# Optimization experiments

Measured on AMD Instinct MI355X. Metric: run time of the kernel, lower is better.

The kernel has to match this reference:

```python
import jax, jax.numpy as jnp
import numpy as np

BATCH = 2048
INPUT_DIM = 256
NUM_SUBCARRIERS = 256
HIDDEN_DIM = 256


def setup_inputs() -> dict:
    key = jax.random.key(0)
    ks = jax.random.split(key, 7)
    C, I, H = NUM_SUBCARRIERS, INPUT_DIM, HIDDEN_DIM
    # PyTorch nn.Linear default init: U(-1/sqrt(fan_in), 1/sqrt(fan_in))
    s1 = 1.0 / np.sqrt(I)
    s2 = 1.0 / np.sqrt(H)
    x = jax.random.normal(ks[0], (BATCH, I), dtype=jnp.float32)
    W1 = jax.random.uniform(ks[1], (C, I, H), jnp.float32, -s1, s1)
    b1 = jax.random.uniform(ks[2], (C, H), jnp.float32, -s1, s1)
    W2 = jax.random.uniform(ks[3], (C, H, H), jnp.float32, -s2, s2)
    b2 = jax.random.uniform(ks[4], (C, H), jnp.float32, -s2, s2)
    W3 = jax.random.uniform(ks[5], (C, H), jnp.float32, -s2, s2)  # [C, H] (out dim 1 squeezed)
    b3 = jax.random.uniform(ks[6], (C,), jnp.float32, -s2, s2)
    return {"x": x, "W1": W1, "b1": b1, "W2": W2, "b2": b2, "W3": W3, "b3": b3}


def reference(x, W1, b1, W2, b2, W3, b3):
    # Stacked (batched) version of the per-subcarrier Python loop:
    # for each subcarrier c: relu(relu(x @ W1[c] + b1[c]) @ W2[c] + b2[c]) @ W3[c] + b3[c]
    h1 = jax.nn.relu(jnp.einsum('bi,cih->cbh', x, W1) + b1[:, None, :])   # [C, B, H]
    h2 = jax.nn.relu(jnp.einsum('cbh,chk->cbk', h1, W2) + b2[:, None, :])  # [C, B, H]
    out = jnp.einsum('cbh,ch->cb', h2, W3) + b3[:, None]                   # [C, B]
    return out.T  # [B, C], matches torch.cat(outputs, dim=1)
```

## Files before the change

### kernel.cpp

```cpp
#include <hip/hip_runtime.h>

typedef unsigned short u16;
using u16x4  = __attribute__((ext_vector_type(4))) unsigned short;
using u16x8  = __attribute__((ext_vector_type(8))) unsigned short;
using bf16x8 = __attribute__((ext_vector_type(8))) short;
using f32x4  = __attribute__((ext_vector_type(4))) float;
using f32x16 = __attribute__((ext_vector_type(16))) float;

__device__ __forceinline__ u16 f2bf(float f) {
  union { float f; unsigned u; } v; v.f = f;
  unsigned r = v.u + 0x7FFFu + ((v.u >> 16) & 1u);
  return (u16)(r >> 16);
}

__device__ __forceinline__ unsigned cvt_pk_bf16(float a, float b) {
  unsigned d;
  asm("v_cvt_pk_bf16_f32 %0, %1, %2" : "=v"(d) : "v"(a), "v"(b));
  return d;
}

__global__ void convert_x_k(const float* __restrict__ in, u16* __restrict__ out) {
  int i = blockIdx.x * 256 + threadIdx.x;
  float4 v = ((const float4*)in)[i];
  u16x4 u;
  u.x = f2bf(v.x); u.y = f2bf(v.y); u.z = f2bf(v.z); u.w = f2bf(v.w);
  ((u16x4*)out)[i] = u;
}

__global__ __launch_bounds__(256) void transpose_w2_k(
    const float* __restrict__ W1, const float* __restrict__ W2,
    u16* __restrict__ w1t, u16* __restrict__ w2t) {
  __shared__ float tile[64][65];
  const int bid = blockIdx.x;
  const int mat = bid >> 4;
  const int tl  = bid & 15;
  const int i0 = (tl >> 2) * 64, h0 = (tl & 3) * 64;
  const float* src = (mat < 256) ? (W1 + mat * 65536) : (W2 + (mat - 256) * 65536);
  u16*       dst   = (mat < 256) ? (w1t + mat * 65536) : (w2t + (mat - 256) * 65536);
  const int t = threadIdx.x;
#pragma unroll
  for (int j = 0; j < 4; ++j) {
    int lin = j * 256 + t;
    int row = lin >> 4, c4 = lin & 15;
    float4 v = *(const float4*)(src + (i0 + row) * 256 + h0 + c4 * 4);
    tile[row][c4 * 4 + 0] = v.x; tile[row][c4 * 4 + 1] = v.y;
    tile[row][c4 * 4 + 2] = v.z; tile[row][c4 * 4 + 3] = v.w;
  }
  __syncthreads();
  const int col = t >> 2;
  const int kk  = (t & 3) * 8;
#pragma unroll
  for (int p = 0; p < 2; ++p) {
    u16x8 o;
#pragma unroll
    for (int jj = 0; jj < 8; ++jj)
      o[jj] = f2bf(tile[p * 32 + kk + jj][col]);
    *(u16x8*)(dst + ((i0 >> 4) + 2 * p + (kk >> 4)) * 4096 + (h0 + col) * 16 + (kk & 8)) = o;
  }
}

__global__ __launch_bounds__(512, 4) void rf_main_k(
    const u16* __restrict__ xb, const u16* __restrict__ w1t, const u16* __restrict__ w2t,
    const float* __restrict__ b1, const float* __restrict__ b2,
    const float* __restrict__ w3, const float* __restrict__ b3,
    float* __restrict__ out) {
  __shared__ u16 sH[128 * 264];
  __shared__ float red[8 * 128];

  const int bid  = blockIdx.x;
  const int xcd  = bid & 7;
  const int j8   = bid >> 3;
  const int c    = xcd * 32 + (j8 >> 4);
  const int b0   = (j8 & 15) * 128;
  const int t    = threadIdx.x;
  const int lane = t & 63;
  const int w    = t >> 6;
  const int l31  = lane & 31;
  const int hi   = lane >> 5;
  const bool hiH = hi != 0;
  const int wq   = w & 3;
  const int bh   = w >> 2;
  const int m_base = wq * 64;
  const int n_base = bh * 64;

  const u16* w1c = w1t + c * 65536;
  const u16* w2c = w2t + c * 65536;
  const int aoff = (m_base + l31) * 16 + hi * 8;
  const int bbase = (n_base + l31) * 264 + hi * 8;
  const int bidx = __builtin_amdgcn_readfirstlane(c * 256 + m_base);

  f32x16 acc[2][2];
  bf16x8 aA[2], aB[2];

#define LOADA(dst, base)                                         \
  { dst[0] = *(const bf16x8*)(base);                             \
    dst[1] = *(const bf16x8*)((base) + 512); }

#define COMPUTE(fr, ch)                                          \
  { bf16x8 _b0 = *(const bf16x8*)&sH[bbase + (ch) * 16];         \
    bf16x8 _b1 = *(const bf16x8*)&sH[bbase + (ch) * 16 + 8448];  \
    acc[0][0] = __builtin_amdgcn_mfma_f32_32x32x16_bf16(fr[0], _b0, acc[0][0], 0, 0, 0); \
    acc[1][0] = __builtin_amdgcn_mfma_f32_32x32x16_bf16(fr[1], _b0, acc[1][0], 0, 0, 0); \
    acc[0][1] = __builtin_amdgcn_mfma_f32_32x32x16_bf16(fr[0], _b1, acc[0][1], 0, 0, 0); \
    acc[1][1] = __builtin_amdgcn_mfma_f32_32x32x16_bf16(fr[1], _b1, acc[1][1], 0, 0, 0); }

#define INIT_ACC(bp)                                             \
  { _Pragma("unroll")                                            \
    for (int _mi = 0; _mi < 2; ++_mi) {                          \
      _Pragma("unroll")                                          \
      for (int _g = 0; _g < 4; ++_g) {                           \
        f32x4 _lo = *(const f32x4*)((bp) + bidx + _mi * 32 + _g * 8);     \
        f32x4 _h4 = *(const f32x4*)((bp) + bidx + _mi * 32 + _g * 8 + 4); \
        _Pragma("unroll")                                        \
        for (int _r = 0; _r < 4; ++_r) {                         \
          float _v = hiH ? _h4[_r] : _lo[_r];                    \
          acc[_mi][0][_g * 4 + _r] = _v;                         \
          acc[_mi][1][_g * 4 + _r] = _v;                         \
        } } } }

  LOADA(aA, w1c + aoff);

#pragma unroll
  for (int i = 0; i < 8; ++i) {
    int flat = i * 512 + t;
    int r = flat >> 5, s = flat & 31;
    u16x8 g = *(const u16x8*)(xb + (b0 + r) * 256 + s * 8);
    *(u16x8*)&sH[r * 264 + s * 8] = g;
  }
  INIT_ACC(b1);
  __syncthreads();

#pragma unroll 1
  for (int ch = 0; ch < 16; ch += 2) {
    LOADA(aB, w1c + (ch + 1) * 4096 + aoff);
    COMPUTE(aA, ch);
    const u16* nxt = (ch == 14) ? (w2c + aoff)
                                : (w1c + (ch + 2) * 4096 + aoff);
    LOADA(aA, nxt);
    COMPUTE(aB, ch + 1);
  }

  __syncthreads();
#pragma unroll
  for (int mi = 0; mi < 2; ++mi)
#pragma unroll
    for (int nj = 0; nj < 2; ++nj) {
      const int row = n_base + nj * 32 + l31;
#pragma unroll
      for (int g = 0; g < 4; ++g) {
        float v0 = fmaxf(acc[mi][nj][g * 4 + 0], 0.f);
        float v1 = fmaxf(acc[mi][nj][g * 4 + 1], 0.f);
        float v2 = fmaxf(acc[mi][nj][g * 4 + 2], 0.f);
        float v3 = fmaxf(acc[mi][nj][g * 4 + 3], 0.f);
        uint2 p;
        p.x = cvt_pk_bf16(v0, v1);
        p.y = cvt_pk_bf16(v2, v3);
        *(uint2*)&sH[row * 264 + m_base + mi * 32 + g * 8 + 4 * hi] = p;
      }
    }
  INIT_ACC(b2);
  __syncthreads();

#pragma unroll 1
  for (int ch = 0; ch < 16; ch += 2) {
    LOADA(aB, w2c + (ch + 1) * 4096 + aoff);
    COMPUTE(aA, ch);
    if (ch < 14) LOADA(aA, w2c + (ch + 2) * 4096 + aoff);
    COMPUTE(aB, ch + 1);
  }

  float part0 = 0.f, part1 = 0.f;
#pragma unroll
  for (int mi = 0; mi < 2; ++mi)
#pragma unroll
    for (int g = 0; g < 4; ++g) {
      f32x4 wlo = *(const f32x4*)(w3 + bidx + mi * 32 + g * 8);
      f32x4 whi = *(const f32x4*)(w3 + bidx + mi * 32 + g * 8 + 4);
#pragma unroll
      for (int r = 0; r < 4; ++r) {
        float wv = hiH ? whi[r] : wlo[r];
        part0 += fmaxf(acc[mi][0][g * 4 + r], 0.f) * wv;
        part1 += fmaxf(acc[mi][1][g * 4 + r], 0.f) * wv;
      }
    }
  red[(wq * 2 + hi) * 128 + n_base + l31]      = part0;
  red[(wq * 2 + hi) * 128 + n_base + 32 + l31] = part1;
  __syncthreads();
  if (t < 128) {
    float v = b3[c];
#pragma unroll
    for (int k = 0; k < 8; ++k) v += red[k * 128 + t];
    out[(b0 + t) * 256 + c] = v;
  }
#undef LOADA
#undef COMPUTE
#undef INIT_ACC
}

extern "C" void kernel_launch(void* const* d_in, const int* in_sizes, int n_in,
                              void* d_out, int out_size, void* d_ws, size_t ws_size,
                              hipStream_t stream) {
  const float* x  = (const float*)d_in[0];
  const float* W1 = (const float*)d_in[1];
  const float* b1 = (const float*)d_in[2];
  const float* W2 = (const float*)d_in[3];
  const float* b2 = (const float*)d_in[4];
  const float* W3 = (const float*)d_in[5];
  const float* b3 = (const float*)d_in[6];
  float* out = (float*)d_out;

  char* ws = (char*)d_ws;
  u16* xb  = (u16*)ws;
  u16* w1t = (u16*)(ws + (1u << 20));
  u16* w2t = (u16*)(ws + (1u << 20) + (32u << 20));

  convert_x_k   <<<512,  256, 0, stream>>>(x,  xb);
  transpose_w2_k<<<8192, 256, 0, stream>>>(W1, W2, w1t, w2t);
  rf_main_k     <<<4096, 512, 0, stream>>>(xb, w1t, w2t, b1, b2, W3, b3, out);
}
```

Baseline: 304.3 us.

## Retile warps to 128x32 output tiles and merge x conversion into weight prepass

Each warp now covers 128 hidden units by 32 batch rows instead of 64x64. It loads four A fragments from global memory and one shared-memory B fragment per step, halving LDS reads for B and the final reduction buffer. This doubles per-warp global A-fragment traffic and register pressure, with the weights reloaded by twice as many warps. Separately, the x conversion kernel is folded into the transpose prepass as extra blocks, which removes one kernel launch.

```diff
diff --git a/kernel.cpp b/kernel.cpp
--- a/kernel.cpp
+++ b/kernel.cpp
@@ -19,25 +19,26 @@
   return d;
 }
 
-__global__ void convert_x_k(const float* __restrict__ in, u16* __restrict__ out) {
-  int i = blockIdx.x * 256 + threadIdx.x;
-  float4 v = ((const float4*)in)[i];
-  u16x4 u;
-  u.x = f2bf(v.x); u.y = f2bf(v.y); u.z = f2bf(v.z); u.w = f2bf(v.w);
-  ((u16x4*)out)[i] = u;
-}
-
-__global__ __launch_bounds__(256) void transpose_w2_k(
+__global__ __launch_bounds__(256) void prepass_k(
     const float* __restrict__ W1, const float* __restrict__ W2,
-    u16* __restrict__ w1t, u16* __restrict__ w2t) {
+    u16* __restrict__ w1t, u16* __restrict__ w2t,
+    const float* __restrict__ x, u16* __restrict__ xb) {
   __shared__ float tile[64][65];
   const int bid = blockIdx.x;
+  const int t = threadIdx.x;
+  if (bid >= 8192) {
+    int i = (bid - 8192) * 256 + t;
+    float4 v = ((const float4*)x)[i];
+    u16x4 u;
+    u.x = f2bf(v.x); u.y = f2bf(v.y); u.z = f2bf(v.z); u.w = f2bf(v.w);
+    ((u16x4*)xb)[i] = u;
+    return;
+  }
   const int mat = bid >> 4;
   const int tl  = bid & 15;
   const int i0 = (tl >> 2) * 64, h0 = (tl & 3) * 64;
   const float* src = (mat < 256) ? (W1 + mat * 65536) : (W2 + (mat - 256) * 65536);
   u16*       dst   = (mat < 256) ? (w1t + mat * 65536) : (w2t + (mat - 256) * 65536);
-  const int t = threadIdx.x;
 #pragma unroll
   for (int j = 0; j < 4; ++j) {
     int lin = j * 256 + t;
@@ -65,7 +66,7 @@
     const float* __restrict__ w3, const float* __restrict__ b3,
     float* __restrict__ out) {
   __shared__ u16 sH[128 * 264];
-  __shared__ float red[8 * 128];
+  __shared__ float red[4 * 128];
 
   const int bid  = blockIdx.x;
   const int xcd  = bid & 7;
@@ -78,10 +79,10 @@
   const int l31  = lane & 31;
   const int hi   = lane >> 5;
   const bool hiH = hi != 0;
-  const int wq   = w & 3;
-  const int bh   = w >> 2;
-  const int m_base = wq * 64;
-  const int n_base = bh * 64;
+  const int wq   = w & 1;
+  const int bh   = w >> 1;
+  const int m_base = wq * 128;
+  const int n_base = bh * 32;
 
   const u16* w1c = w1t + c * 65536;
   const u16* w2c = w2t + c * 65536;
@@ -89,34 +90,32 @@
   const int bbase = (n_base + l31) * 264 + hi * 8;
   const int bidx = __builtin_amdgcn_readfirstlane(c * 256 + m_base);
 
-  f32x16 acc[2][2];
-  bf16x8 aA[2], aB[2];
+  f32x16 acc[4];
+  bf16x8 aA[4], aB[4];
 
 #define LOADA(dst, base)                                         \
-  { dst[0] = *(const bf16x8*)(base);                             \
-    dst[1] = *(const bf16x8*)((base) + 512); }
+  { _Pragma("unroll")                                            \
+    for (int _mi = 0; _mi < 4; ++_mi)                            \
+      dst[_mi] = *(const bf16x8*)((base) + _mi * 512); }
 
 #define COMPUTE(fr, ch)                                          \
-  { bf16x8 _b0 = *(const bf16x8*)&sH[bbase + (ch) * 16];         \
-    bf16x8 _b1 = *(const bf16x8*)&sH[bbase + (ch) * 16 + 8448];  \
-    acc[0][0] = __builtin_amdgcn_mfma_f32_32x32x16_bf16(fr[0], _b0, acc[0][0], 0, 0, 0); \
-    acc[1][0] = __builtin_amdgcn_mfma_f32_32x32x16_bf16(fr[1], _b0, acc[1][0], 0, 0, 0); \
-    acc[0][1] = __builtin_amdgcn_mfma_f32_32x32x16_bf16(fr[0], _b1, acc[0][1], 0, 0, 0); \
-    acc[1][1] = __builtin_amdgcn_mfma_f32_32x32x16_bf16(fr[1], _b1, acc[1][1], 0, 0, 0); }
+  { bf16x8 _b = *(const bf16x8*)&sH[bbase + (ch) * 16];          \
+    acc[0] = __builtin_amdgcn_mfma_f32_32x32x16_bf16(fr[0], _b, acc[0], 0, 0, 0); \
+    acc[1] = __builtin_amdgcn_mfma_f32_32x32x16_bf16(fr[1], _b, acc[1], 0, 0, 0); \
+    acc[2] = __builtin_amdgcn_mfma_f32_32x32x16_bf16(fr[2], _b, acc[2], 0, 0, 0); \
+    acc[3] = __builtin_amdgcn_mfma_f32_32x32x16_bf16(fr[3], _b, acc[3], 0, 0, 0); }
 
 #define INIT_ACC(bp)                                             \
   { _Pragma("unroll")                                            \
-    for (int _mi = 0; _mi < 2; ++_mi) {                          \
+    for (int _mi = 0; _mi < 4; ++_mi) {                          \
       _Pragma("unroll")                                          \
       for (int _g = 0; _g < 4; ++_g) {                           \
         f32x4 _lo = *(const f32x4*)((bp) + bidx + _mi * 32 + _g * 8);     \
         f32x4 _h4 = *(const f32x4*)((bp) + bidx + _mi * 32 + _g * 8 + 4); \
         _Pragma("unroll")                                        \
-        for (int _r = 0; _r < 4; ++_r) {                         \
-          float _v = hiH ? _h4[_r] : _lo[_r];                    \
-          acc[_mi][0][_g * 4 + _r] = _v;                         \
-          acc[_mi][1][_g * 4 + _r] = _v;                         \
-        } } } }
+        for (int _r = 0; _r < 4; ++_r)                           \
+          acc[_mi][_g * 4 + _r] = hiH ? _h4[_r] : _lo[_r];       \
+      } } }
 
   LOADA(aA, w1c + aoff);
 
@@ -141,23 +140,22 @@
   }
 
   __syncthreads();
-#pragma unroll
-  for (int mi = 0; mi < 2; ++mi)
-#pragma unroll
-    for (int nj = 0; nj < 2; ++nj) {
-      const int row = n_base + nj * 32 + l31;
+  {
+    const int row = n_base + l31;
+#pragma unroll
+    for (int mi = 0; mi < 4; ++mi)
 #pragma unroll
       for (int g = 0; g < 4; ++g) {
-        float v0 = fmaxf(acc[mi][nj][g * 4 + 0], 0.f);
-        float v1 = fmaxf(acc[mi][nj][g * 4 + 1], 0.f);
-        float v2 = fmaxf(acc[mi][nj][g * 4 + 2], 0.f);
-        float v3 = fmaxf(acc[mi][nj][g * 4 + 3], 0.f);
+        float v0 = fmaxf(acc[mi][g * 4 + 0], 0.f);
+        float v1 = fmaxf(acc[mi][g * 4 + 1], 0.f);
+        float v2 = fmaxf(acc[mi][g * 4 + 2], 0.f);
+        float v3 = fmaxf(acc[mi][g * 4 + 3], 0.f);
         uint2 p;
         p.x = cvt_pk_bf16(v0, v1);
         p.y = cvt_pk_bf16(v2, v3);
         *(uint2*)&sH[row * 264 + m_base + mi * 32 + g * 8 + 4 * hi] = p;
       }
-    }
+  }
   INIT_ACC(b2);
   __syncthreads();
 
@@ -169,9 +167,9 @@
     COMPUTE(aB, ch + 1);
   }
 
-  float part0 = 0.f, part1 = 0.f;
-#pragma unroll
-  for (int mi = 0; mi < 2; ++mi)
+  float part = 0.f;
+#pragma unroll
+  for (int mi = 0; mi < 4; ++mi)
 #pragma unroll
     for (int g = 0; g < 4; ++g) {
       f32x4 wlo = *(const f32x4*)(w3 + bidx + mi * 32 + g * 8);
@@ -179,17 +177,15 @@
 #pragma unroll
       for (int r = 0; r < 4; ++r) {
         float wv = hiH ? whi[r] : wlo[r];
-        part0 += fmaxf(acc[mi][0][g * 4 + r], 0.f) * wv;
-        part1 += fmaxf(acc[mi][1][g * 4 + r], 0.f) * wv;
+        part += fmaxf(acc[mi][g * 4 + r], 0.f) * wv;
       }
     }
-  red[(wq * 2 + hi) * 128 + n_base + l31]      = part0;
-  red[(wq * 2 + hi) * 128 + n_base + 32 + l31] = part1;
+  red[(wq * 2 + hi) * 128 + n_base + l31] = part;
   __syncthreads();
   if (t < 128) {
     float v = b3[c];
 #pragma unroll
-    for (int k = 0; k < 8; ++k) v += red[k * 128 + t];
+    for (int k = 0; k < 4; ++k) v += red[k * 128 + t];
     out[(b0 + t) * 256 + c] = v;
   }
 #undef LOADA
@@ -214,7 +210,6 @@
   u16* w1t = (u16*)(ws + (1u << 20));
   u16* w2t = (u16*)(ws + (1u << 20) + (32u << 20));
 
-  convert_x_k   <<<512,  256, 0, stream>>>(x,  xb);
-  transpose_w2_k<<<8192, 256, 0, stream>>>(W1, W2, w1t, w2t);
-  rf_main_k     <<<4096, 512, 0, stream>>>(xb, w1t, w2t, b1, b2, W3, b3, out);
-}
+  prepass_k <<<8704, 256, 0, stream>>>(W1, W2, w1t, w2t, x, xb);
+  rf_main_k <<<4096, 512, 0, stream>>>(xb, w1t, w2t, b1, b2, W3, b3, out);
+}
```

Result: slower. 343.0 us (+12.7%).

## Double batch tile per block, prefetch LDS B fragments, merge prepass kernels

Applied to the files above, without the earlier changes.

Each main-kernel block now handles 256 batch rows instead of 128, so each wave computes a 64x128 tile and the per-subcarrier weight fragments are reused across twice as many rows. Global weight traffic and block count are halved. B operands are now double-buffered from LDS in registers ahead of the MFMAs. The x conversion and weight transpose are fused into one launch to drop a kernel launch. Costs: more accumulator registers and LDS per block, which lowers occupancy (launch bounds reduced to 2 blocks per CU).

```diff
diff --git a/kernel.cpp b/kernel.cpp
--- a/kernel.cpp
+++ b/kernel.cpp
@@ -19,25 +19,26 @@
   return d;
 }
 
-__global__ void convert_x_k(const float* __restrict__ in, u16* __restrict__ out) {
-  int i = blockIdx.x * 256 + threadIdx.x;
-  float4 v = ((const float4*)in)[i];
-  u16x4 u;
-  u.x = f2bf(v.x); u.y = f2bf(v.y); u.z = f2bf(v.z); u.w = f2bf(v.w);
-  ((u16x4*)out)[i] = u;
-}
-
-__global__ __launch_bounds__(256) void transpose_w2_k(
+__global__ __launch_bounds__(256) void prepass_k(
     const float* __restrict__ W1, const float* __restrict__ W2,
-    u16* __restrict__ w1t, u16* __restrict__ w2t) {
+    u16* __restrict__ w1t, u16* __restrict__ w2t,
+    const float* __restrict__ x, u16* __restrict__ xb) {
   __shared__ float tile[64][65];
   const int bid = blockIdx.x;
+  const int t = threadIdx.x;
+  if (bid >= 8192) {
+    int i = (bid - 8192) * 256 + t;
+    float4 v = ((const float4*)x)[i];
+    u16x4 u;
+    u.x = f2bf(v.x); u.y = f2bf(v.y); u.z = f2bf(v.z); u.w = f2bf(v.w);
+    ((u16x4*)xb)[i] = u;
+    return;
+  }
   const int mat = bid >> 4;
   const int tl  = bid & 15;
   const int i0 = (tl >> 2) * 64, h0 = (tl & 3) * 64;
   const float* src = (mat < 256) ? (W1 + mat * 65536) : (W2 + (mat - 256) * 65536);
   u16*       dst   = (mat < 256) ? (w1t + mat * 65536) : (w2t + (mat - 256) * 65536);
-  const int t = threadIdx.x;
 #pragma unroll
   for (int j = 0; j < 4; ++j) {
     int lin = j * 256 + t;
@@ -59,19 +60,18 @@
   }
 }
 
-__global__ __launch_bounds__(512, 4) void rf_main_k(
+__global__ __launch_bounds__(512, 2) void rf_main_k(
     const u16* __restrict__ xb, const u16* __restrict__ w1t, const u16* __restrict__ w2t,
     const float* __restrict__ b1, const float* __restrict__ b2,
     const float* __restrict__ w3, const float* __restrict__ b3,
     float* __restrict__ out) {
-  __shared__ u16 sH[128 * 264];
-  __shared__ float red[8 * 128];
+  __shared__ u16 sH[256 * 264];
 
   const int bid  = blockIdx.x;
   const int xcd  = bid & 7;
   const int j8   = bid >> 3;
-  const int c    = xcd * 32 + (j8 >> 4);
-  const int b0   = (j8 & 15) * 128;
+  const int c    = xcd * 32 + (j8 >> 3);
+  const int b0   = (j8 & 7) * 256;
   const int t    = threadIdx.x;
   const int lane = t & 63;
   const int w    = t >> 6;
@@ -81,28 +81,34 @@
   const int wq   = w & 3;
   const int bh   = w >> 2;
   const int m_base = wq * 64;
-  const int n_base = bh * 64;
 
   const u16* w1c = w1t + c * 65536;
   const u16* w2c = w2t + c * 65536;
   const int aoff = (m_base + l31) * 16 + hi * 8;
-  const int bbase = (n_base + l31) * 264 + hi * 8;
+  int bb[4];
+#pragma unroll
+  for (int nj = 0; nj < 4; ++nj)
+    bb[nj] = (bh * 128 + nj * 32 + l31) * 264 + hi * 8;
   const int bidx = __builtin_amdgcn_readfirstlane(c * 256 + m_base);
 
-  f32x16 acc[2][2];
-  bf16x8 aA[2], aB[2];
+  f32x16 acc[2][4];
+  bf16x8 aA[2], aB[2], bX[4], bY[4];
 
 #define LOADA(dst, base)                                         \
   { dst[0] = *(const bf16x8*)(base);                             \
     dst[1] = *(const bf16x8*)((base) + 512); }
 
-#define COMPUTE(fr, ch)                                          \
-  { bf16x8 _b0 = *(const bf16x8*)&sH[bbase + (ch) * 16];         \
-    bf16x8 _b1 = *(const bf16x8*)&sH[bbase + (ch) * 16 + 8448];  \
-    acc[0][0] = __builtin_amdgcn_mfma_f32_32x32x16_bf16(fr[0], _b0, acc[0][0], 0, 0, 0); \
-    acc[1][0] = __builtin_amdgcn_mfma_f32_32x32x16_bf16(fr[1], _b0, acc[1][0], 0, 0, 0); \
-    acc[0][1] = __builtin_amdgcn_mfma_f32_32x32x16_bf16(fr[0], _b1, acc[0][1], 0, 0, 0); \
-    acc[1][1] = __builtin_amdgcn_mfma_f32_32x32x16_bf16(fr[1], _b1, acc[1][1], 0, 0, 0); }
+#define LOADB(dst, ch)                                           \
+  { _Pragma("unroll")                                            \
+    for (int _nj = 0; _nj < 4; ++_nj)                            \
+      dst[_nj] = *(const bf16x8*)&sH[bb[_nj] + (ch) * 16]; }
+
+#define COMPUTE(afr, bfr)                                        \
+  { _Pragma("unroll")                                            \
+    for (int _nj = 0; _nj < 4; ++_nj) {                          \
+      acc[0][_nj] = __builtin_amdgcn_mfma_f32_32x32x16_bf16(afr[0], bfr[_nj], acc[0][_nj], 0, 0, 0); \
+      acc[1][_nj] = __builtin_amdgcn_mfma_f32_32x32x16_bf16(afr[1], bfr[_nj], acc[1][_nj], 0, 0, 0); \
+    } }
 
 #define INIT_ACC(bp)                                             \
   { _Pragma("unroll")                                            \
@@ -114,14 +120,15 @@
         _Pragma("unroll")                                        \
         for (int _r = 0; _r < 4; ++_r) {                         \
           float _v = hiH ? _h4[_r] : _lo[_r];                    \
-          acc[_mi][0][_g * 4 + _r] = _v;                         \
-          acc[_mi][1][_g * 4 + _r] = _v;                         \
+          _Pragma("unroll")                                      \
+          for (int _nj = 0; _nj < 4; ++_nj)                      \
+            acc[_mi][_nj][_g * 4 + _r] = _v;                     \
         } } } }
 
   LOADA(aA, w1c + aoff);
 
 #pragma unroll
-  for (int i = 0; i < 8; ++i) {
+  for (int i = 0; i < 16; ++i) {
     int flat = i * 512 + t;
     int r = flat >> 5, s = flat & 31;
     u16x8 g = *(const u16x8*)(xb + (b0 + r) * 256 + s * 8);
@@ -130,22 +137,25 @@
   INIT_ACC(b1);
   __syncthreads();
 
+  LOADB(bX, 0);
 #pragma unroll 1
   for (int ch = 0; ch < 16; ch += 2) {
     LOADA(aB, w1c + (ch + 1) * 4096 + aoff);
-    COMPUTE(aA, ch);
+    LOADB(bY, ch + 1);
+    COMPUTE(aA, bX);
     const u16* nxt = (ch == 14) ? (w2c + aoff)
                                 : (w1c + (ch + 2) * 4096 + aoff);
     LOADA(aA, nxt);
-    COMPUTE(aB, ch + 1);
-  }
-
-  __syncthreads();
-#pragma unroll
-  for (int mi = 0; mi < 2; ++mi)
-#pragma unroll
-    for (int nj = 0; nj < 2; ++nj) {
-      const int row = n_base + nj * 32 + l31;
+    if (ch < 14) LOADB(bX, ch + 2);
+    COMPUTE(aB, bY);
+  }
+
+  __syncthreads();
+#pragma unroll
+  for (int nj = 0; nj < 4; ++nj) {
+    const int row = bh * 128 + nj * 32 + l31;
+#pragma unroll
+    for (int mi = 0; mi < 2; ++mi)
 #pragma unroll
       for (int g = 0; g < 4; ++g) {
         float v0 = fmaxf(acc[mi][nj][g * 4 + 0], 0.f);
@@ -157,19 +167,24 @@
         p.y = cvt_pk_bf16(v2, v3);
         *(uint2*)&sH[row * 264 + m_base + mi * 32 + g * 8 + 4 * hi] = p;
       }
-    }
+  }
   INIT_ACC(b2);
   __syncthreads();
 
+  LOADB(bX, 0);
 #pragma unroll 1
   for (int ch = 0; ch < 16; ch += 2) {
     LOADA(aB, w2c + (ch + 1) * 4096 + aoff);
-    COMPUTE(aA, ch);
-    if (ch < 14) LOADA(aA, w2c + (ch + 2) * 4096 + aoff);
-    COMPUTE(aB, ch + 1);
-  }
-
-  float part0 = 0.f, part1 = 0.f;
+    LOADB(bY, ch + 1);
+    COMPUTE(aA, bX);
+    if (ch < 14) {
+      LOADA(aA, w2c + (ch + 2) * 4096 + aoff);
+      LOADB(bX, ch + 2);
+    }
+    COMPUTE(aB, bY);
+  }
+
+  float part[4] = {0.f, 0.f, 0.f, 0.f};
 #pragma unroll
   for (int mi = 0; mi < 2; ++mi)
 #pragma unroll
@@ -179,20 +194,25 @@
 #pragma unroll
       for (int r = 0; r < 4; ++r) {
         float wv = hiH ? whi[r] : wlo[r];
-        part0 += fmaxf(acc[mi][0][g * 4 + r], 0.f) * wv;
-        part1 += fmaxf(acc[mi][1][g * 4 + r], 0.f) * wv;
+#pragma unroll
+        for (int nj = 0; nj < 4; ++nj)
+          part[nj] += fmaxf(acc[mi][nj][g * 4 + r], 0.f) * wv;
       }
     }
-  red[(wq * 2 + hi) * 128 + n_base + l31]      = part0;
-  red[(wq * 2 + hi) * 128 + n_base + 32 + l31] = part1;
-  __syncthreads();
-  if (t < 128) {
+  __syncthreads();
+  float* red = (float*)sH;
+#pragma unroll
+  for (int nj = 0; nj < 4; ++nj)
+    red[(wq * 2 + hi) * 256 + bh * 128 + nj * 32 + l31] = part[nj];
+  __syncthreads();
+  if (t < 256) {
     float v = b3[c];
 #pragma unroll
-    for (int k = 0; k < 8; ++k) v += red[k * 128 + t];
+    for (int k = 0; k < 8; ++k) v += red[k * 256 + t];
     out[(b0 + t) * 256 + c] = v;
   }
 #undef LOADA
+#undef LOADB
 #undef COMPUTE
 #undef INIT_ACC
 }
@@ -214,7 +234,6 @@
   u16* w1t = (u16*)(ws + (1u << 20));
   u16* w2t = (u16*)(ws + (1u << 20) + (32u << 20));
 
-  convert_x_k   <<<512,  256, 0, stream>>>(x,  xb);
-  transpose_w2_k<<<8192, 256, 0, stream>>>(W1, W2, w1t, w2t);
-  rf_main_k     <<<4096, 512, 0, stream>>>(xb, w1t, w2t, b1, b2, W3, b3, out);
-}
+  prepass_k <<<8704, 256, 0, stream>>>(W1, W2, w1t, w2t, x, xb);
+  rf_main_k <<<2048, 512, 0, stream>>>(xb, w1t, w2t, b1, b2, W3, b3, out);
+}
```

After: 302.3 us. About the same (-0.6%).

## Triple-buffer weight fragments, prefetch LDS operands, merge prepass kernels

Applied to the files above, without the earlier changes.

The main kernel's chunk loops are now fully unrolled. A-fragments from global memory are rotated through a three-deep register buffer, loaded two chunks ahead, and B-fragments from LDS are double-buffered one chunk ahead. MFMA groups are wrapped in s_setprio to favour issuing matrix instructions. The x conversion and the weight transpose are fused into a single prepass launch to drop one kernel launch. The cost is higher register pressure at 4 waves/SIMD occupancy and a larger unrolled code body.

```diff
diff --git a/kernel.cpp b/kernel.cpp
--- a/kernel.cpp
+++ b/kernel.cpp
@@ -19,25 +19,26 @@
   return d;
 }
 
-__global__ void convert_x_k(const float* __restrict__ in, u16* __restrict__ out) {
-  int i = blockIdx.x * 256 + threadIdx.x;
-  float4 v = ((const float4*)in)[i];
-  u16x4 u;
-  u.x = f2bf(v.x); u.y = f2bf(v.y); u.z = f2bf(v.z); u.w = f2bf(v.w);
-  ((u16x4*)out)[i] = u;
-}
-
-__global__ __launch_bounds__(256) void transpose_w2_k(
+__global__ __launch_bounds__(256) void prepass_k(
     const float* __restrict__ W1, const float* __restrict__ W2,
-    u16* __restrict__ w1t, u16* __restrict__ w2t) {
+    u16* __restrict__ w1t, u16* __restrict__ w2t,
+    const float* __restrict__ x, u16* __restrict__ xb) {
   __shared__ float tile[64][65];
   const int bid = blockIdx.x;
+  const int t = threadIdx.x;
+  if (bid >= 8192) {
+    int i = (bid - 8192) * 256 + t;
+    float4 v = ((const float4*)x)[i];
+    u16x4 u;
+    u.x = f2bf(v.x); u.y = f2bf(v.y); u.z = f2bf(v.z); u.w = f2bf(v.w);
+    ((u16x4*)xb)[i] = u;
+    return;
+  }
   const int mat = bid >> 4;
   const int tl  = bid & 15;
   const int i0 = (tl >> 2) * 64, h0 = (tl & 3) * 64;
   const float* src = (mat < 256) ? (W1 + mat * 65536) : (W2 + (mat - 256) * 65536);
   u16*       dst   = (mat < 256) ? (w1t + mat * 65536) : (w2t + (mat - 256) * 65536);
-  const int t = threadIdx.x;
 #pragma unroll
   for (int j = 0; j < 4; ++j) {
     int lin = j * 256 + t;
@@ -85,24 +86,29 @@
 
   const u16* w1c = w1t + c * 65536;
   const u16* w2c = w2t + c * 65536;
-  const int aoff = (m_base + l31) * 16 + hi * 8;
+  const int aoff  = (m_base + l31) * 16 + hi * 8;
   const int bbase = (n_base + l31) * 264 + hi * 8;
-  const int bidx = __builtin_amdgcn_readfirstlane(c * 256 + m_base);
+  const int bidx  = __builtin_amdgcn_readfirstlane(c * 256 + m_base);
 
   f32x16 acc[2][2];
-  bf16x8 aA[2], aB[2];
+  bf16x8 aS[3][2];
+  bf16x8 bS[2][2];
 
 #define LOADA(dst, base)                                         \
   { dst[0] = *(const bf16x8*)(base);                             \
     dst[1] = *(const bf16x8*)((base) + 512); }
 
-#define COMPUTE(fr, ch)                                          \
-  { bf16x8 _b0 = *(const bf16x8*)&sH[bbase + (ch) * 16];         \
-    bf16x8 _b1 = *(const bf16x8*)&sH[bbase + (ch) * 16 + 8448];  \
-    acc[0][0] = __builtin_amdgcn_mfma_f32_32x32x16_bf16(fr[0], _b0, acc[0][0], 0, 0, 0); \
-    acc[1][0] = __builtin_amdgcn_mfma_f32_32x32x16_bf16(fr[1], _b0, acc[1][0], 0, 0, 0); \
-    acc[0][1] = __builtin_amdgcn_mfma_f32_32x32x16_bf16(fr[0], _b1, acc[0][1], 0, 0, 0); \
-    acc[1][1] = __builtin_amdgcn_mfma_f32_32x32x16_bf16(fr[1], _b1, acc[1][1], 0, 0, 0); }
+#define LOADB(dst, ch)                                           \
+  { dst[0] = *(const bf16x8*)&sH[bbase + (ch) * 16];             \
+    dst[1] = *(const bf16x8*)&sH[bbase + (ch) * 16 + 8448]; }
+
+#define COMPUTE(afr, bfr)                                        \
+  { __builtin_amdgcn_s_setprio(1);                               \
+    acc[0][0] = __builtin_amdgcn_mfma_f32_32x32x16_bf16(afr[0], bfr[0], acc[0][0], 0, 0, 0); \
+    acc[1][0] = __builtin_amdgcn_mfma_f32_32x32x16_bf16(afr[1], bfr[0], acc[1][0], 0, 0, 0); \
+    acc[0][1] = __builtin_amdgcn_mfma_f32_32x32x16_bf16(afr[0], bfr[1], acc[0][1], 0, 0, 0); \
+    acc[1][1] = __builtin_amdgcn_mfma_f32_32x32x16_bf16(afr[1], bfr[1], acc[1][1], 0, 0, 0); \
+    __builtin_amdgcn_s_setprio(0); }
 
 #define INIT_ACC(bp)                                             \
   { _Pragma("unroll")                                            \
@@ -118,7 +124,8 @@
           acc[_mi][1][_g * 4 + _r] = _v;                         \
         } } } }
 
-  LOADA(aA, w1c + aoff);
+  LOADA(aS[0], w1c + 0 * 4096 + aoff);
+  LOADA(aS[1], w1c + 1 * 4096 + aoff);
 
 #pragma unroll
   for (int i = 0; i < 8; ++i) {
@@ -130,14 +137,13 @@
   INIT_ACC(b1);
   __syncthreads();
 
-#pragma unroll 1
-  for (int ch = 0; ch < 16; ch += 2) {
-    LOADA(aB, w1c + (ch + 1) * 4096 + aoff);
-    COMPUTE(aA, ch);
-    const u16* nxt = (ch == 14) ? (w2c + aoff)
-                                : (w1c + (ch + 2) * 4096 + aoff);
-    LOADA(aA, nxt);
-    COMPUTE(aB, ch + 1);
+  LOADB(bS[0], 0);
+#pragma unroll
+  for (int ch = 0; ch < 16; ++ch) {
+    const u16* ab = (ch + 2 < 16) ? (w1c + (ch + 2) * 4096) : (w2c + (ch - 14) * 4096);
+    LOADA(aS[(ch + 2) % 3], ab + aoff);
+    if (ch + 1 < 16) LOADB(bS[(ch + 1) & 1], ch + 1);
+    COMPUTE(aS[ch % 3], bS[ch & 1]);
   }
 
   __syncthreads();
@@ -161,12 +167,12 @@
   INIT_ACC(b2);
   __syncthreads();
 
-#pragma unroll 1
-  for (int ch = 0; ch < 16; ch += 2) {
-    LOADA(aB, w2c + (ch + 1) * 4096 + aoff);
-    COMPUTE(aA, ch);
-    if (ch < 14) LOADA(aA, w2c + (ch + 2) * 4096 + aoff);
-    COMPUTE(aB, ch + 1);
+  LOADB(bS[0], 0);
+#pragma unroll
+  for (int ch = 0; ch < 16; ++ch) {
+    if (ch + 2 < 16) LOADA(aS[ch % 3], w2c + (ch + 2) * 4096 + aoff);
+    if (ch + 1 < 16) LOADB(bS[(ch + 1) & 1], ch + 1);
+    COMPUTE(aS[(ch + 1) % 3], bS[ch & 1]);
   }
 
   float part0 = 0.f, part1 = 0.f;
@@ -193,6 +199,7 @@
     out[(b0 + t) * 256 + c] = v;
   }
 #undef LOADA
+#undef LOADB
 #undef COMPUTE
 #undef INIT_ACC
 }
@@ -214,7 +221,6 @@
   u16* w1t = (u16*)(ws + (1u << 20));
   u16* w2t = (u16*)(ws + (1u << 20) + (32u << 20));
 
-  convert_x_k   <<<512,  256, 0, stream>>>(x,  xb);
-  transpose_w2_k<<<8192, 256, 0, stream>>>(W1, W2, w1t, w2t);
-  rf_main_k     <<<4096, 512, 0, stream>>>(xb, w1t, w2t, b1, b2, W3, b3, out);
-}
+  prepass_k <<<8704, 256, 0, stream>>>(W1, W2, w1t, w2t, x, xb);
+  rf_main_k <<<4096, 512, 0, stream>>>(xb, w1t, w2t, b1, b2, W3, b3, out);
+}
```

New measurement: 307.1 us. Within noise of the previous version (+0.9%).
